# Performance work log

Hardware: AMD Instinct MI355X
Metric: run time of the kernel (lower is better)

The kernel has to match this reference:

```python
import jax, jax.numpy as jnp
import numpy as np

N_NODES = 50000


def setup_inputs() -> dict:
    key = jax.random.key(0)
    ks = jax.random.split(key, 10)
    B, N, D, H, O = 2, N_NODES, 128, 128, 10
    x = jax.random.normal(ks[0], (B, N, D), dtype=jnp.float32)
    edge_index = jax.random.randint(ks[1], (2, 800000), 0, N, dtype=jnp.int32)
    s = lambda fan_in: 1.0 / np.sqrt(fan_in)
    W  = jax.random.uniform(ks[2], (D, H), jnp.float32, -s(D), s(D))
    b  = jnp.zeros((H,), jnp.float32)
    W1 = jax.random.uniform(ks[3], (H, H // 2), jnp.float32, -s(H), s(H))
    b1 = jnp.zeros((H // 2,), jnp.float32)
    W2 = jax.random.uniform(ks[4], (H // 2, H // 4), jnp.float32, -s(H // 2), s(H // 2))
    b2 = jnp.zeros((H // 4,), jnp.float32)
    W3 = jax.random.uniform(ks[5], (H // 4, O), jnp.float32, -s(H // 4), s(H // 4))
    b3 = jnp.zeros((O,), jnp.float32)
    return {"x": x, "edge_index": edge_index, "W": W, "b": b,
            "W1": W1, "b1": b1, "W2": W2, "b2": b2, "W3": W3, "b3": b3}


def reference(x, edge_index, W, b, W1, b1, W2, b2, W3, b3):
    # GraphConvolution (Kipf): support = x @ W; out[dst] += support[src]; + b
    src, dst = edge_index[0], edge_index[1]
    support = jnp.einsum("bnd,dh->bnh", x, W)          # [B, N, H]
    msgs = support[:, src, :]                            # [B, E, H] gather
    agg = jnp.zeros_like(support).at[:, dst, :].add(msgs)  # scatter-add
    h = jax.nn.gelu(agg + b, approximate=False)          # GELU (torch default erf)
    # dropout is identity at inference (training=False)
    h = jax.nn.relu(jnp.einsum("bnh,hk->bnk", h, W1) + b1)
    h = jax.nn.relu(jnp.einsum("bnk,km->bnm", h, W2) + b2)
    h = jnp.einsum("bnm,mo->bno", h, W3) + b3            # [B, N, O]
    return h.mean(axis=1)                                # [B, O]
```

## Files before the change

### kernel.cpp

```cpp
#include <hip/hip_runtime.h>
#include <math.h>

#define NN 50000
#define DD 128
#define HH 128
#define L1 64
#define L2 32
#define OO 10

__device__ __forceinline__ float bf2f_lo(unsigned u) { return __uint_as_float(u << 16); }
__device__ __forceinline__ float bf2f_hi(unsigned u) { return __uint_as_float(u & 0xffff0000u); }
__device__ __forceinline__ unsigned short f2bf(float f) {
    unsigned u = __float_as_uint(f);
    return (unsigned short)((u + 0x7fffu + ((u >> 16) & 1u)) >> 16);
}

__global__ __launch_bounds__(256) void k_support(
    const float* __restrict__ x, const float* __restrict__ W,
    unsigned short* __restrict__ supb, int rows,
    const int* __restrict__ ei, int* __restrict__ counts, int E)
{
    __shared__ float xs[64][DD];
    __shared__ float wh[64][HH];
    const int tid = threadIdx.x;
    const int row0 = blockIdx.x * 64;

    for (int u = tid * 4; u < 64 * DD; u += 256 * 4) {
        const int r = u >> 7, c = u & 127;
        float4 v = make_float4(0.f, 0.f, 0.f, 0.f);
        if (row0 + r < rows) v = *(const float4*)(x + (size_t)(row0 + r) * DD + c);
        *(float4*)(&xs[r][c]) = v;
    }

    {
        const int chunk = (E + gridDim.x - 1) / gridDim.x;
        const int e0 = blockIdx.x * chunk;
        const int e1 = min(e0 + chunk, E);
        for (int e = e0 + tid; e < e1; e += 256)
            atomicAdd(&counts[ei[(size_t)E + e]], 1);
    }

    const int cg = tid & 31;
    const int rg = tid >> 5;
    float4 acc[8];
    #pragma unroll
    for (int i = 0; i < 8; ++i) acc[i] = make_float4(0.f, 0.f, 0.f, 0.f);

    for (int p = 0; p < 2; ++p) {
        __syncthreads();
        for (int u = tid * 4; u < 64 * HH; u += 256 * 4) {
            const int r = u >> 7, c = u & 127;
            *(float4*)(&wh[r][c]) = *(const float4*)(W + (size_t)(p * 64 + r) * HH + c);
        }
        __syncthreads();
        #pragma unroll 2
        for (int k = 0; k < 64; k += 4) {
            float4 wv[4];
            #pragma unroll
            for (int jj = 0; jj < 4; ++jj) wv[jj] = *(const float4*)(&wh[k + jj][cg * 4]);
            #pragma unroll
            for (int q = 0; q < 2; ++q) {
                #pragma unroll
                for (int i = 0; i < 4; ++i) {
                    const float4 xv = *(const float4*)(&xs[q * 32 + rg * 4 + i][p * 64 + k]);
                    float4* a = &acc[q * 4 + i];
                    a->x = fmaf(xv.x, wv[0].x, fmaf(xv.y, wv[1].x, fmaf(xv.z, wv[2].x, fmaf(xv.w, wv[3].x, a->x))));
                    a->y = fmaf(xv.x, wv[0].y, fmaf(xv.y, wv[1].y, fmaf(xv.z, wv[2].y, fmaf(xv.w, wv[3].y, a->y))));
                    a->z = fmaf(xv.x, wv[0].z, fmaf(xv.y, wv[1].z, fmaf(xv.z, wv[2].z, fmaf(xv.w, wv[3].z, a->z))));
                    a->w = fmaf(xv.x, wv[0].w, fmaf(xv.y, wv[1].w, fmaf(xv.z, wv[2].w, fmaf(xv.w, wv[3].w, a->w))));
                }
            }
        }
    }

    #pragma unroll
    for (int q = 0; q < 2; ++q)
        #pragma unroll
        for (int i = 0; i < 4; ++i) {
            const int r = row0 + q * 32 + rg * 4 + i;
            if (r < rows) {
                const float4 a = acc[q * 4 + i];
                ushort4 o;
                o.x = f2bf(a.x); o.y = f2bf(a.y); o.z = f2bf(a.z); o.w = f2bf(a.w);
                *(ushort4*)(supb + (size_t)r * HH + cg * 4) = o;
            }
        }
}

__global__ __launch_bounds__(1024) void k_scan1(
    const int* __restrict__ counts, int* __restrict__ offsets,
    int* __restrict__ blksum, int n)
{
    __shared__ int wsum[16], woff[16];
    const int tid = threadIdx.x, lane = tid & 63, wv = tid >> 6;
    const int i = blockIdx.x * 1024 + tid;
    int v = (i < n) ? counts[i] : 0;
    int x = v;
    #pragma unroll
    for (int d = 1; d < 64; d <<= 1) { int t = __shfl_up(x, d); if (lane >= d) x += t; }
    if (lane == 63) wsum[wv] = x;
    __syncthreads();
    if (wv == 0 && lane < 16) {
        int y = wsum[lane];
        #pragma unroll
        for (int d = 1; d < 16; d <<= 1) { int t = __shfl_up(y, d); if (lane >= d) y += t; }
        woff[lane] = y - wsum[lane];
        if (lane == 15) blksum[blockIdx.x] = y;
    }
    __syncthreads();
    if (i < n) offsets[i] = woff[wv] + (x - v);
}

__global__ __launch_bounds__(1024) void k_scan2(
    int* __restrict__ offsets, const int* __restrict__ blksum, int nblk, int n)
{
    __shared__ int base_sh, tot_sh;
    const int tid = threadIdx.x, lane = tid & 63, wv = tid >> 6;
    if (wv == 0) {
        int v = (lane < nblk) ? blksum[lane] : 0;
        int x = v;
        #pragma unroll
        for (int d = 1; d < 64; d <<= 1) { int t = __shfl_up(x, d); if (lane >= d) x += t; }
        int incl = __shfl(x, blockIdx.x);
        int own  = __shfl(v, blockIdx.x);
        int tot  = __shfl(x, nblk - 1);
        if (lane == 0) { base_sh = incl - own; tot_sh = tot; }
    }
    __syncthreads();
    const int i = blockIdx.x * 1024 + tid;
    if (i < n) offsets[i] += base_sh;
    if (blockIdx.x == nblk - 1 && tid == 0) offsets[n] = tot_sh;
}

__global__ __launch_bounds__(256) void k_bucket(
    const int* __restrict__ ei, const int* __restrict__ offsets,
    int* __restrict__ cursor, int* __restrict__ ss, int E)
{
    int e = blockIdx.x * 256 + threadIdx.x;
    if (e < E) {
        int d = ei[E + e];
        int pos = offsets[d] + atomicAdd(&cursor[d], 1);
        ss[pos] = ei[e];
    }
}

__global__ __launch_bounds__(256) void k_agg(
    const unsigned short* __restrict__ supb, const int* __restrict__ offsets,
    const int* __restrict__ ss, unsigned short* __restrict__ aggb, int nn)
{
    const int tid = threadIdx.x;
    const int lane = tid & 63;
    const int wv = tid >> 6;
    const int d = blockIdx.x * 4 + wv;
    if (d >= nn) return;
    const int b = lane >> 5;
    const int f = lane & 31;
    const size_t bbase = (size_t)b * nn * HH;
    const unsigned short* sp = supb + bbase + f * 4;
    const int s0 = offsets[d], s1 = offsets[d + 1];
    float4 a = make_float4(0.f, 0.f, 0.f, 0.f);
    float4 a2 = make_float4(0.f, 0.f, 0.f, 0.f);
    int i = s0;
    for (; i + 2 <= s1; i += 2) {
        const int sA = ss[i], sB = ss[i + 1];
        const uint2 rA = *(const uint2*)(sp + (size_t)sA * HH);
        const uint2 rB = *(const uint2*)(sp + (size_t)sB * HH);
        a.x  += bf2f_lo(rA.x); a.y  += bf2f_hi(rA.x); a.z  += bf2f_lo(rA.y); a.w  += bf2f_hi(rA.y);
        a2.x += bf2f_lo(rB.x); a2.y += bf2f_hi(rB.x); a2.z += bf2f_lo(rB.y); a2.w += bf2f_hi(rB.y);
    }
    if (i < s1) {
        const uint2 r = *(const uint2*)(sp + (size_t)ss[i] * HH);
        a.x += bf2f_lo(r.x); a.y += bf2f_hi(r.x); a.z += bf2f_lo(r.y); a.w += bf2f_hi(r.y);
    }
    a.x += a2.x; a.y += a2.y; a.z += a2.z; a.w += a2.w;
    ushort4 o;
    o.x = f2bf(a.x); o.y = f2bf(a.y); o.z = f2bf(a.z); o.w = f2bf(a.w);
    *(ushort4*)(aggb + bbase + (size_t)d * HH + f * 4) = o;
}

__global__ __launch_bounds__(256) void k_scatter(
    const int* __restrict__ ei, const unsigned short* __restrict__ supb,
    float* __restrict__ aggf, int E, int B)
{
    const int tid = threadIdx.x;
    const int eg = tid >> 5;
    const int t4 = (tid & 31) << 2;
    const int e = blockIdx.x * 8 + eg;
    if (e >= E) return;
    const int src = ei[e];
    const int dst = ei[E + e];
    for (int b = 0; b < B; ++b) {
        const uint2 r = *(const uint2*)(supb + ((size_t)b * NN + src) * HH + t4);
        float* ap = aggf + ((size_t)b * NN + dst) * HH + t4;
        unsafeAtomicAdd(ap + 0, bf2f_lo(r.x));
        unsafeAtomicAdd(ap + 1, bf2f_hi(r.x));
        unsafeAtomicAdd(ap + 2, bf2f_lo(r.y));
        unsafeAtomicAdd(ap + 3, bf2f_hi(r.y));
    }
}

__global__ __launch_bounds__(256) void k_cvt(
    const float* __restrict__ in, unsigned short* __restrict__ outb, int n)
{
    int i = blockIdx.x * 256 + threadIdx.x;
    if (i < n) outb[i] = f2bf(in[i]);
}

__global__ __launch_bounds__(512) void k_mlp(
    const unsigned short* __restrict__ aggb, const float* __restrict__ b0v,
    const float* __restrict__ W1, const float* __restrict__ b1v,
    const float* __restrict__ W2, const float* __restrict__ b2v,
    float* __restrict__ partials, int rows)
{
    __shared__ float w1s[HH][L1];
    __shared__ float w2s[L1][L2];
    __shared__ float hs[64 * 136];
    __shared__ float b0s[DD], b1s[L1], b2s[L2];
    __shared__ float oacc[64];

    const int tid = threadIdx.x;
    const int row0 = blockIdx.x * 64;

    for (int u = tid * 4; u < HH * L1; u += 2048)
        *(float4*)(&w1s[u >> 6][u & 63]) = *(const float4*)(W1 + u);
    for (int u = tid * 4; u < L1 * L2; u += 2048)
        *(float4*)(&w2s[u >> 5][u & 31]) = *(const float4*)(W2 + u);
    if (tid < DD) b0s[tid] = b0v[tid];
    if (tid < L1) b1s[tid] = b1v[tid];
    if (tid < L2) b2s[tid] = b2v[tid];
    if (tid < 64) oacc[tid] = 0.f;
    __syncthreads();

    for (int u = tid * 8; u < 64 * DD; u += 512 * 8) {
        const int r = u >> 7, c = u & 127;
        float4 g0 = make_float4(0.f, 0.f, 0.f, 0.f);
        float4 g1 = g0;
        if (row0 + r < rows) {
            const uint4 raw = *(const uint4*)(aggb + (size_t)(row0 + r) * HH + c);
            float v[8];
            v[0] = bf2f_lo(raw.x) + b0s[c + 0]; v[1] = bf2f_hi(raw.x) + b0s[c + 1];
            v[2] = bf2f_lo(raw.y) + b0s[c + 2]; v[3] = bf2f_hi(raw.y) + b0s[c + 3];
            v[4] = bf2f_lo(raw.z) + b0s[c + 4]; v[5] = bf2f_hi(raw.z) + b0s[c + 5];
            v[6] = bf2f_lo(raw.w) + b0s[c + 6]; v[7] = bf2f_hi(raw.w) + b0s[c + 7];
            #pragma unroll
            for (int t = 0; t < 8; ++t) v[t] = 0.5f * v[t] * (1.f + erff(v[t] * 0.70710678118654752f));
            g0 = make_float4(v[0], v[1], v[2], v[3]);
            g1 = make_float4(v[4], v[5], v[6], v[7]);
        }
        *(float4*)(&hs[r * 136 + c]) = g0;
        *(float4*)(&hs[r * 136 + c + 4]) = g1;
    }
    __syncthreads();

    const int cg = tid & 15;
    const int rg = tid >> 4;
    float4 acc0 = *(const float4*)(&b1s[cg * 4]);
    float4 acc1 = acc0;
    #pragma unroll 4
    for (int j = 0; j < HH; j += 4) {
        float4 wv[4];
        #pragma unroll
        for (int jj = 0; jj < 4; ++jj) wv[jj] = *(const float4*)(&w1s[j + jj][cg * 4]);
        const float4 h0 = *(const float4*)(&hs[(rg * 2 + 0) * 136 + j]);
        const float4 h1 = *(const float4*)(&hs[(rg * 2 + 1) * 136 + j]);
        acc0.x = fmaf(h0.x, wv[0].x, fmaf(h0.y, wv[1].x, fmaf(h0.z, wv[2].x, fmaf(h0.w, wv[3].x, acc0.x))));
        acc0.y = fmaf(h0.x, wv[0].y, fmaf(h0.y, wv[1].y, fmaf(h0.z, wv[2].y, fmaf(h0.w, wv[3].y, acc0.y))));
        acc0.z = fmaf(h0.x, wv[0].z, fmaf(h0.y, wv[1].z, fmaf(h0.z, wv[2].z, fmaf(h0.w, wv[3].z, acc0.z))));
        acc0.w = fmaf(h0.x, wv[0].w, fmaf(h0.y, wv[1].w, fmaf(h0.z, wv[2].w, fmaf(h0.w, wv[3].w, acc0.w))));
        acc1.x = fmaf(h1.x, wv[0].x, fmaf(h1.y, wv[1].x, fmaf(h1.z, wv[2].x, fmaf(h1.w, wv[3].x, acc1.x))));
        acc1.y = fmaf(h1.x, wv[0].y, fmaf(h1.y, wv[1].y, fmaf(h1.z, wv[2].y, fmaf(h1.w, wv[3].y, acc1.y))));
        acc1.z = fmaf(h1.x, wv[0].z, fmaf(h1.y, wv[1].z, fmaf(h1.z, wv[2].z, fmaf(h1.w, wv[3].z, acc1.z))));
        acc1.w = fmaf(h1.x, wv[0].w, fmaf(h1.y, wv[1].w, fmaf(h1.z, wv[2].w, fmaf(h1.w, wv[3].w, acc1.w))));
    }
    acc0.x = fmaxf(acc0.x, 0.f); acc0.y = fmaxf(acc0.y, 0.f);
    acc0.z = fmaxf(acc0.z, 0.f); acc0.w = fmaxf(acc0.w, 0.f);
    acc1.x = fmaxf(acc1.x, 0.f); acc1.y = fmaxf(acc1.y, 0.f);
    acc1.z = fmaxf(acc1.z, 0.f); acc1.w = fmaxf(acc1.w, 0.f);
    __syncthreads();
    float* h1p = hs;
    *(float4*)(&h1p[(rg * 2 + 0) * 68 + cg * 4]) = acc0;
    *(float4*)(&h1p[(rg * 2 + 1) * 68 + cg * 4]) = acc1;
    __syncthreads();

    float* h2p = hs + 5120;
    {
        const int cg2 = tid & 7;
        const int r2 = tid >> 3;
        float4 a = *(const float4*)(&b2s[cg2 * 4]);
        #pragma unroll 4
        for (int j = 0; j < L1; j += 4) {
            float4 wv[4];
            #pragma unroll
            for (int jj = 0; jj < 4; ++jj) wv[jj] = *(const float4*)(&w2s[j + jj][cg2 * 4]);
            const float4 hv = *(const float4*)(&h1p[r2 * 68 + j]);
            a.x = fmaf(hv.x, wv[0].x, fmaf(hv.y, wv[1].x, fmaf(hv.z, wv[2].x, fmaf(hv.w, wv[3].x, a.x))));
            a.y = fmaf(hv.x, wv[0].y, fmaf(hv.y, wv[1].y, fmaf(hv.z, wv[2].y, fmaf(hv.w, wv[3].y, a.y))));
            a.z = fmaf(hv.x, wv[0].z, fmaf(hv.y, wv[1].z, fmaf(hv.z, wv[2].z, fmaf(hv.w, wv[3].z, a.z))));
            a.w = fmaf(hv.x, wv[0].w, fmaf(hv.y, wv[1].w, fmaf(hv.z, wv[2].w, fmaf(hv.w, wv[3].w, a.w))));
        }
        a.x = fmaxf(a.x, 0.f); a.y = fmaxf(a.y, 0.f);
        a.z = fmaxf(a.z, 0.f); a.w = fmaxf(a.w, 0.f);
        __syncthreads();
        *(float4*)(&h2p[r2 * 36 + cg2 * 4]) = a;
    }
    __syncthreads();

    {
        const int c = tid & 31;
        const int g = tid >> 5;
        float p0 = 0.f, p1 = 0.f;
        #pragma unroll
        for (int i = 0; i < 4; ++i) {
            const int r = g * 4 + i;
            const int grow = row0 + r;
            if (grow < rows) {
                const float v = h2p[r * 36 + c];
                if (grow >= NN) p1 += v; else p0 += v;
            }
        }
        if (p0 != 0.f) atomicAdd(&oacc[c], p0);
        if (p1 != 0.f) atomicAdd(&oacc[32 + c], p1);
    }
    __syncthreads();
    if (tid < 64) partials[(size_t)blockIdx.x * 64 + tid] = oacc[tid];
}

__global__ __launch_bounds__(256) void k_reduce(
    const float* __restrict__ partials, float* __restrict__ accum, int nblk)
{
    __shared__ float lsum[4][64];
    const int t = threadIdx.x & 63;
    const int w = threadIdx.x >> 6;
    float s = 0.f;
    for (int g = blockIdx.x * 4 + w; g < nblk; g += gridDim.x * 4)
        s += partials[(size_t)g * 64 + t];
    lsum[w][t] = s;
    __syncthreads();
    if (threadIdx.x < 64) {
        const float v = lsum[0][t] + lsum[1][t] + lsum[2][t] + lsum[3][t];
        unsafeAtomicAdd(&accum[t], v);
    }
}

__global__ __launch_bounds__(64) void k_final(
    const float* __restrict__ accum, const float* __restrict__ W3,
    const float* __restrict__ b3v, float* __restrict__ out)
{
    const int tid = threadIdx.x;
    if (tid < 2 * OO) {
        const int b = tid / OO, o = tid % OO;
        float acc = b3v[o];
        const float inv = 1.0f / (float)NN;
        #pragma unroll
        for (int j = 0; j < L2; ++j) acc += (accum[b * 32 + j] * inv) * W3[j * OO + o];
        out[tid] = acc;
    }
}

extern "C" void kernel_launch(void* const* d_in, const int* in_sizes, int n_in,
                              void* d_out, int out_size, void* d_ws, size_t ws_size,
                              hipStream_t stream) {
    const float* x  = (const float*)d_in[0];
    const int*   ei = (const int*)d_in[1];
    const float* W  = (const float*)d_in[2];
    const float* b0 = (const float*)d_in[3];
    const float* W1 = (const float*)d_in[4];
    const float* b1 = (const float*)d_in[5];
    const float* W2 = (const float*)d_in[6];
    const float* b2 = (const float*)d_in[7];
    const float* W3 = (const float*)d_in[8];
    const float* b3 = (const float*)d_in[9];
    float* out = (float*)d_out;

    const int B = in_sizes[0] / (NN * DD);
    const int E = in_sizes[1] / 2;
    const int rows = B * NN;
    const int nblk_mlp = (rows + 63) / 64;
    const int nsb = (NN + 1023) / 1024;

    unsigned short* supb = (unsigned short*)d_ws;
    unsigned short* aggb = supb + (size_t)rows * HH;
    float* partials = (float*)(aggb + (size_t)rows * HH);
    float* accum    = partials + (size_t)nblk_mlp * 64;
    int*   counts   = (int*)(accum + 64);
    int*   cursor   = counts + NN;
    int*   offsets  = cursor + NN;
    int*   blksum   = offsets + NN + 1;
    int*   ss       = blksum + 64;
    const size_t need = ((size_t)rows * HH * 2) * sizeof(unsigned short)
                      + ((size_t)nblk_mlp * 64 + 64) * sizeof(float)
                      + ((size_t)NN * 3 + 1 + 64 + E) * sizeof(int);

    if (ws_size >= need && nsb <= 64) {
        hipMemsetAsync(accum, 0, (64 + 2 * (size_t)NN) * sizeof(int), stream);
        k_support<<<dim3(nblk_mlp), dim3(256), 0, stream>>>(x, W, supb, rows, ei, counts, E);
        k_scan1<<<dim3(nsb), dim3(1024), 0, stream>>>(counts, offsets, blksum, NN);
        k_scan2<<<dim3(nsb), dim3(1024), 0, stream>>>(offsets, blksum, nsb, NN);
        k_bucket<<<dim3((E + 255) / 256), dim3(256), 0, stream>>>(ei, offsets, cursor, ss, E);
        k_agg<<<dim3((NN + 3) / 4), dim3(256), 0, stream>>>(supb, offsets, ss, aggb, NN);
    } else {
        float* aggf = (float*)counts;
        hipMemsetAsync(accum, 0, 64 * sizeof(float), stream);
        hipMemsetAsync(aggf, 0, (size_t)rows * HH * sizeof(float), stream);
        k_support<<<dim3(nblk_mlp), dim3(256), 0, stream>>>(x, W, supb, rows, ei, (int*)aggf, 0);
        k_scatter<<<dim3((E + 7) / 8), dim3(256), 0, stream>>>(ei, supb, aggf, E, B);
        k_cvt<<<dim3((rows * HH + 255) / 256), dim3(256), 0, stream>>>(aggf, aggb, rows * HH);
    }

    k_mlp<<<dim3(nblk_mlp), dim3(512), 0, stream>>>(aggb, b0, W1, b1, W2, b2, partials, rows);
    k_reduce<<<dim3(64), dim3(256), 0, stream>>>(partials, accum, nblk_mlp);
    k_final<<<dim3(1), dim3(64), 0, stream>>>(accum, W3, b3, out);
}
```

Before: 322.0 us.

## Fuse CSR aggregation with GELU and MLP; read W directly in support GEMM

The CSR gather-aggregation now writes GELU activations straight into shared memory and runs the two hidden MLP layers plus the partial mean in the same kernel. This removes the bf16 agg buffer round trip through global memory and one kernel launch. The support GEMM also drops its shared-memory staging of W and reads W from global (L1/L2-cached) memory, with a launch-bounds occupancy hint, which frees LDS. The fused kernel is larger, so fewer blocks may fit per CU and gather latency may be harder to hide. The fallback path now feeds fp32 agg directly into the MLP instead of converting to bf16 first.

After: 363.5 us. 12.9% more time.

```diff
diff --git a/kernel.cpp b/kernel.cpp
--- a/kernel.cpp
+++ b/kernel.cpp
@@ -14,14 +14,16 @@
     unsigned u = __float_as_uint(f);
     return (unsigned short)((u + 0x7fffu + ((u >> 16) & 1u)) >> 16);
 }
-
-__global__ __launch_bounds__(256) void k_support(
+__device__ __forceinline__ float gelu_f(float v) {
+    return 0.5f * v * (1.f + erff(v * 0.70710678118654752f));
+}
+
+__global__ __launch_bounds__(256, 4) void k_support(
     const float* __restrict__ x, const float* __restrict__ W,
     unsigned short* __restrict__ supb, int rows,
     const int* __restrict__ ei, int* __restrict__ counts, int E)
 {
     __shared__ float xs[64][DD];
-    __shared__ float wh[64][HH];
     const int tid = threadIdx.x;
     const int row0 = blockIdx.x * 64;
 
@@ -45,30 +47,24 @@
     float4 acc[8];
     #pragma unroll
     for (int i = 0; i < 8; ++i) acc[i] = make_float4(0.f, 0.f, 0.f, 0.f);
-
-    for (int p = 0; p < 2; ++p) {
-        __syncthreads();
-        for (int u = tid * 4; u < 64 * HH; u += 256 * 4) {
-            const int r = u >> 7, c = u & 127;
-            *(float4*)(&wh[r][c]) = *(const float4*)(W + (size_t)(p * 64 + r) * HH + c);
-        }
-        __syncthreads();
-        #pragma unroll 2
-        for (int k = 0; k < 64; k += 4) {
-            float4 wv[4];
+    __syncthreads();
+
+    const float* wp = W + cg * 4;
+    #pragma unroll 2
+    for (int k = 0; k < DD; k += 4) {
+        float4 wv[4];
+        #pragma unroll
+        for (int jj = 0; jj < 4; ++jj) wv[jj] = *(const float4*)(wp + (size_t)(k + jj) * HH);
+        #pragma unroll
+        for (int q = 0; q < 2; ++q) {
             #pragma unroll
-            for (int jj = 0; jj < 4; ++jj) wv[jj] = *(const float4*)(&wh[k + jj][cg * 4]);
-            #pragma unroll
-            for (int q = 0; q < 2; ++q) {
-                #pragma unroll
-                for (int i = 0; i < 4; ++i) {
-                    const float4 xv = *(const float4*)(&xs[q * 32 + rg * 4 + i][p * 64 + k]);
-                    float4* a = &acc[q * 4 + i];
-                    a->x = fmaf(xv.x, wv[0].x, fmaf(xv.y, wv[1].x, fmaf(xv.z, wv[2].x, fmaf(xv.w, wv[3].x, a->x))));
-                    a->y = fmaf(xv.x, wv[0].y, fmaf(xv.y, wv[1].y, fmaf(xv.z, wv[2].y, fmaf(xv.w, wv[3].y, a->y))));
-                    a->z = fmaf(xv.x, wv[0].z, fmaf(xv.y, wv[1].z, fmaf(xv.z, wv[2].z, fmaf(xv.w, wv[3].z, a->z))));
-                    a->w = fmaf(xv.x, wv[0].w, fmaf(xv.y, wv[1].w, fmaf(xv.z, wv[2].w, fmaf(xv.w, wv[3].w, a->w))));
-                }
+            for (int i = 0; i < 4; ++i) {
+                const float4 xv = *(const float4*)(&xs[q * 32 + rg * 4 + i][k]);
+                float4* a = &acc[q * 4 + i];
+                a->x = fmaf(xv.x, wv[0].x, fmaf(xv.y, wv[1].x, fmaf(xv.z, wv[2].x, fmaf(xv.w, wv[3].x, a->x))));
+                a->y = fmaf(xv.x, wv[0].y, fmaf(xv.y, wv[1].y, fmaf(xv.z, wv[2].y, fmaf(xv.w, wv[3].y, a->y))));
+                a->z = fmaf(xv.x, wv[0].z, fmaf(xv.y, wv[1].z, fmaf(xv.z, wv[2].z, fmaf(xv.w, wv[3].z, a->z))));
+                a->w = fmaf(xv.x, wv[0].w, fmaf(xv.y, wv[1].w, fmaf(xv.z, wv[2].w, fmaf(xv.w, wv[3].w, a->w))));
             }
         }
     }
@@ -144,38 +140,140 @@
     }
 }
 
-__global__ __launch_bounds__(256) void k_agg(
+__global__ __launch_bounds__(512) void k_aggmlp(
     const unsigned short* __restrict__ supb, const int* __restrict__ offsets,
-    const int* __restrict__ ss, unsigned short* __restrict__ aggb, int nn)
-{
+    const int* __restrict__ ss, const float* __restrict__ b0v,
+    const float* __restrict__ W1, const float* __restrict__ b1v,
+    const float* __restrict__ W2, const float* __restrict__ b2v,
+    float* __restrict__ partials, int nn)
+{
+    __shared__ float w1s[HH][L1];
+    __shared__ float w2s[L1][L2];
+    __shared__ float hs[64 * 136];
+    __shared__ float b0s[DD], b1s[L1], b2s[L2];
+    __shared__ float oacc[64];
+
     const int tid = threadIdx.x;
-    const int lane = tid & 63;
-    const int wv = tid >> 6;
-    const int d = blockIdx.x * 4 + wv;
-    if (d >= nn) return;
-    const int b = lane >> 5;
-    const int f = lane & 31;
-    const size_t bbase = (size_t)b * nn * HH;
-    const unsigned short* sp = supb + bbase + f * 4;
-    const int s0 = offsets[d], s1 = offsets[d + 1];
-    float4 a = make_float4(0.f, 0.f, 0.f, 0.f);
-    float4 a2 = make_float4(0.f, 0.f, 0.f, 0.f);
-    int i = s0;
-    for (; i + 2 <= s1; i += 2) {
-        const int sA = ss[i], sB = ss[i + 1];
-        const uint2 rA = *(const uint2*)(sp + (size_t)sA * HH);
-        const uint2 rB = *(const uint2*)(sp + (size_t)sB * HH);
-        a.x  += bf2f_lo(rA.x); a.y  += bf2f_hi(rA.x); a.z  += bf2f_lo(rA.y); a.w  += bf2f_hi(rA.y);
-        a2.x += bf2f_lo(rB.x); a2.y += bf2f_hi(rB.x); a2.z += bf2f_lo(rB.y); a2.w += bf2f_hi(rB.y);
-    }
-    if (i < s1) {
-        const uint2 r = *(const uint2*)(sp + (size_t)ss[i] * HH);
-        a.x += bf2f_lo(r.x); a.y += bf2f_hi(r.x); a.z += bf2f_lo(r.y); a.w += bf2f_hi(r.y);
-    }
-    a.x += a2.x; a.y += a2.y; a.z += a2.z; a.w += a2.w;
-    ushort4 o;
-    o.x = f2bf(a.x); o.y = f2bf(a.y); o.z = f2bf(a.z); o.w = f2bf(a.w);
-    *(ushort4*)(aggb + bbase + (size_t)d * HH + f * 4) = o;
+    const int d0 = blockIdx.x * 32;
+
+    for (int u = tid * 4; u < HH * L1; u += 2048)
+        *(float4*)(&w1s[u >> 6][u & 63]) = *(const float4*)(W1 + u);
+    for (int u = tid * 4; u < L1 * L2; u += 2048)
+        *(float4*)(&w2s[u >> 5][u & 31]) = *(const float4*)(W2 + u);
+    if (tid < DD) b0s[tid] = b0v[tid];
+    if (tid < L1) b1s[tid] = b1v[tid];
+    if (tid < L2) b2s[tid] = b2v[tid];
+    if (tid < 64) oacc[tid] = 0.f;
+    __syncthreads();
+
+    {
+        const int lane = tid & 63;
+        const int wv = tid >> 6;
+        const int b = lane >> 5;
+        const int f = lane & 31;
+        const unsigned short* sp = supb + (size_t)b * nn * HH + f * 4;
+        #pragma unroll
+        for (int i4 = 0; i4 < 4; ++i4) {
+            const int dl = wv * 4 + i4;
+            const int d = d0 + dl;
+            float4 a = make_float4(0.f, 0.f, 0.f, 0.f);
+            float4 a2 = make_float4(0.f, 0.f, 0.f, 0.f);
+            if (d < nn) {
+                const int s0 = offsets[d], s1 = offsets[d + 1];
+                int i = s0;
+                for (; i + 2 <= s1; i += 2) {
+                    const int sA = ss[i], sB = ss[i + 1];
+                    const uint2 rA = *(const uint2*)(sp + (size_t)sA * HH);
+                    const uint2 rB = *(const uint2*)(sp + (size_t)sB * HH);
+                    a.x  += bf2f_lo(rA.x); a.y  += bf2f_hi(rA.x); a.z  += bf2f_lo(rA.y); a.w  += bf2f_hi(rA.y);
+                    a2.x += bf2f_lo(rB.x); a2.y += bf2f_hi(rB.x); a2.z += bf2f_lo(rB.y); a2.w += bf2f_hi(rB.y);
+                }
+                if (i < s1) {
+                    const uint2 r = *(const uint2*)(sp + (size_t)ss[i] * HH);
+                    a.x += bf2f_lo(r.x); a.y += bf2f_hi(r.x); a.z += bf2f_lo(r.y); a.w += bf2f_hi(r.y);
+                }
+            }
+            const float4 bb = *(const float4*)(&b0s[f * 4]);
+            float4 g;
+            g.x = gelu_f(a.x + a2.x + bb.x);
+            g.y = gelu_f(a.y + a2.y + bb.y);
+            g.z = gelu_f(a.z + a2.z + bb.z);
+            g.w = gelu_f(a.w + a2.w + bb.w);
+            *(float4*)(&hs[(b * 32 + dl) * 136 + f * 4]) = g;
+        }
+    }
+    __syncthreads();
+
+    const int cg = tid & 15;
+    const int rg = tid >> 4;
+    float4 acc0 = *(const float4*)(&b1s[cg * 4]);
+    float4 acc1 = acc0;
+    #pragma unroll 4
+    for (int j = 0; j < HH; j += 4) {
+        float4 wv[4];
+        #pragma unroll
+        for (int jj = 0; jj < 4; ++jj) wv[jj] = *(const float4*)(&w1s[j + jj][cg * 4]);
+        const float4 h0 = *(const float4*)(&hs[(rg * 2 + 0) * 136 + j]);
+        const float4 h1 = *(const float4*)(&hs[(rg * 2 + 1) * 136 + j]);
+        acc0.x = fmaf(h0.x, wv[0].x, fmaf(h0.y, wv[1].x, fmaf(h0.z, wv[2].x, fmaf(h0.w, wv[3].x, acc0.x))));
+        acc0.y = fmaf(h0.x, wv[0].y, fmaf(h0.y, wv[1].y, fmaf(h0.z, wv[2].y, fmaf(h0.w, wv[3].y, acc0.y))));
+        acc0.z = fmaf(h0.x, wv[0].z, fmaf(h0.y, wv[1].z, fmaf(h0.z, wv[2].z, fmaf(h0.w, wv[3].z, acc0.z))));
+        acc0.w = fmaf(h0.x, wv[0].w, fmaf(h0.y, wv[1].w, fmaf(h0.z, wv[2].w, fmaf(h0.w, wv[3].w, acc0.w))));
+        acc1.x = fmaf(h1.x, wv[0].x, fmaf(h1.y, wv[1].x, fmaf(h1.z, wv[2].x, fmaf(h1.w, wv[3].x, acc1.x))));
+        acc1.y = fmaf(h1.x, wv[0].y, fmaf(h1.y, wv[1].y, fmaf(h1.z, wv[2].y, fmaf(h1.w, wv[3].y, acc1.y))));
+        acc1.z = fmaf(h1.x, wv[0].z, fmaf(h1.y, wv[1].z, fmaf(h1.z, wv[2].z, fmaf(h1.w, wv[3].z, acc1.z))));
+        acc1.w = fmaf(h1.x, wv[0].w, fmaf(h1.y, wv[1].w, fmaf(h1.z, wv[2].w, fmaf(h1.w, wv[3].w, acc1.w))));
+    }
+    acc0.x = fmaxf(acc0.x, 0.f); acc0.y = fmaxf(acc0.y, 0.f);
+    acc0.z = fmaxf(acc0.z, 0.f); acc0.w = fmaxf(acc0.w, 0.f);
+    acc1.x = fmaxf(acc1.x, 0.f); acc1.y = fmaxf(acc1.y, 0.f);
+    acc1.z = fmaxf(acc1.z, 0.f); acc1.w = fmaxf(acc1.w, 0.f);
+    __syncthreads();
+    float* h1p = hs;
+    *(float4*)(&h1p[(rg * 2 + 0) * 68 + cg * 4]) = acc0;
+    *(float4*)(&h1p[(rg * 2 + 1) * 68 + cg * 4]) = acc1;
+    __syncthreads();
+
+    float* h2p = hs + 5120;
+    {
+        const int cg2 = tid & 7;
+        const int r2 = tid >> 3;
+        float4 a = *(const float4*)(&b2s[cg2 * 4]);
+        #pragma unroll 4
+        for (int j = 0; j < L1; j += 4) {
+            float4 wv[4];
+            #pragma unroll
+            for (int jj = 0; jj < 4; ++jj) wv[jj] = *(const float4*)(&w2s[j + jj][cg2 * 4]);
+            const float4 hv = *(const float4*)(&h1p[r2 * 68 + j]);
+            a.x = fmaf(hv.x, wv[0].x, fmaf(hv.y, wv[1].x, fmaf(hv.z, wv[2].x, fmaf(hv.w, wv[3].x, a.x))));
+            a.y = fmaf(hv.x, wv[0].y, fmaf(hv.y, wv[1].y, fmaf(hv.z, wv[2].y, fmaf(hv.w, wv[3].y, a.y))));
+            a.z = fmaf(hv.x, wv[0].z, fmaf(hv.y, wv[1].z, fmaf(hv.z, wv[2].z, fmaf(hv.w, wv[3].z, a.z))));
+            a.w = fmaf(hv.x, wv[0].w, fmaf(hv.y, wv[1].w, fmaf(hv.z, wv[2].w, fmaf(hv.w, wv[3].w, a.w))));
+        }
+        a.x = fmaxf(a.x, 0.f); a.y = fmaxf(a.y, 0.f);
+        a.z = fmaxf(a.z, 0.f); a.w = fmaxf(a.w, 0.f);
+        __syncthreads();
+        *(float4*)(&h2p[r2 * 36 + cg2 * 4]) = a;
+    }
+    __syncthreads();
+
+    {
+        const int c = tid & 31;
+        const int g = tid >> 5;
+        float p0 = 0.f, p1 = 0.f;
+        #pragma unroll
+        for (int i = 0; i < 4; ++i) {
+            const int r = g * 4 + i;
+            if (d0 + (r & 31) < nn) {
+                const float v = h2p[r * 36 + c];
+                if (r >= 32) p1 += v; else p0 += v;
+            }
+        }
+        if (p0 != 0.f) atomicAdd(&oacc[c], p0);
+        if (p1 != 0.f) atomicAdd(&oacc[32 + c], p1);
+    }
+    __syncthreads();
+    if (tid < 64) partials[(size_t)blockIdx.x * 64 + tid] = oacc[tid];
 }
 
 __global__ __launch_bounds__(256) void k_scatter(
@@ -199,15 +297,8 @@
     }
 }
 
-__global__ __launch_bounds__(256) void k_cvt(
-    const float* __restrict__ in, unsigned short* __restrict__ outb, int n)
-{
-    int i = blockIdx.x * 256 + threadIdx.x;
-    if (i < n) outb[i] = f2bf(in[i]);
-}
-
-__global__ __launch_bounds__(512) void k_mlp(
-    const unsigned short* __restrict__ aggb, const float* __restrict__ b0v,
+__global__ __launch_bounds__(512) void k_mlp_g(
+    const float* __restrict__ aggf, const float* __restrict__ b0v,
     const float* __restrict__ W1, const float* __restrict__ b1v,
     const float* __restrict__ W2, const float* __restrict__ b2v,
     float* __restrict__ partials, int rows)
@@ -231,24 +322,15 @@
     if (tid < 64) oacc[tid] = 0.f;
     __syncthreads();
 
-    for (int u = tid * 8; u < 64 * DD; u += 512 * 8) {
+    for (int u = tid * 4; u < 64 * DD; u += 2048) {
         const int r = u >> 7, c = u & 127;
-        float4 g0 = make_float4(0.f, 0.f, 0.f, 0.f);
-        float4 g1 = g0;
+        float4 g = make_float4(0.f, 0.f, 0.f, 0.f);
         if (row0 + r < rows) {
-            const uint4 raw = *(const uint4*)(aggb + (size_t)(row0 + r) * HH + c);
-            float v[8];
-            v[0] = bf2f_lo(raw.x) + b0s[c + 0]; v[1] = bf2f_hi(raw.x) + b0s[c + 1];
-            v[2] = bf2f_lo(raw.y) + b0s[c + 2]; v[3] = bf2f_hi(raw.y) + b0s[c + 3];
-            v[4] = bf2f_lo(raw.z) + b0s[c + 4]; v[5] = bf2f_hi(raw.z) + b0s[c + 5];
-            v[6] = bf2f_lo(raw.w) + b0s[c + 6]; v[7] = bf2f_hi(raw.w) + b0s[c + 7];
-            #pragma unroll
-            for (int t = 0; t < 8; ++t) v[t] = 0.5f * v[t] * (1.f + erff(v[t] * 0.70710678118654752f));
-            g0 = make_float4(v[0], v[1], v[2], v[3]);
-            g1 = make_float4(v[4], v[5], v[6], v[7]);
-        }
-        *(float4*)(&hs[r * 136 + c]) = g0;
-        *(float4*)(&hs[r * 136 + c + 4]) = g1;
+            const float4 v = *(const float4*)(aggf + (size_t)(row0 + r) * HH + c);
+            g.x = gelu_f(v.x + b0s[c + 0]); g.y = gelu_f(v.y + b0s[c + 1]);
+            g.z = gelu_f(v.z + b0s[c + 2]); g.w = gelu_f(v.w + b0s[c + 3]);
+        }
+        *(float4*)(&hs[r * 136 + c]) = g;
     }
     __syncthreads();
 
@@ -256,7 +338,6 @@
     const int rg = tid >> 4;
     float4 acc0 = *(const float4*)(&b1s[cg * 4]);
     float4 acc1 = acc0;
-    #pragma unroll 4
     for (int j = 0; j < HH; j += 4) {
         float4 wv[4];
         #pragma unroll
@@ -287,7 +368,6 @@
         const int cg2 = tid & 7;
         const int r2 = tid >> 3;
         float4 a = *(const float4*)(&b2s[cg2 * 4]);
-        #pragma unroll 4
         for (int j = 0; j < L1; j += 4) {
             float4 wv[4];
             #pragma unroll
@@ -375,39 +455,38 @@
     const int B = in_sizes[0] / (NN * DD);
     const int E = in_sizes[1] / 2;
     const int rows = B * NN;
-    const int nblk_mlp = (rows + 63) / 64;
+    const int nblk = (NN + 31) / 32;
     const int nsb = (NN + 1023) / 1024;
 
     unsigned short* supb = (unsigned short*)d_ws;
-    unsigned short* aggb = supb + (size_t)rows * HH;
-    float* partials = (float*)(aggb + (size_t)rows * HH);
-    float* accum    = partials + (size_t)nblk_mlp * 64;
+    float* partials = (float*)(supb + (size_t)rows * HH);
+    float* accum    = partials + (size_t)nblk * 64;
     int*   counts   = (int*)(accum + 64);
     int*   cursor   = counts + NN;
     int*   offsets  = cursor + NN;
     int*   blksum   = offsets + NN + 1;
     int*   ss       = blksum + 64;
-    const size_t need = ((size_t)rows * HH * 2) * sizeof(unsigned short)
-                      + ((size_t)nblk_mlp * 64 + 64) * sizeof(float)
+    float* aggf     = (float*)(ss + E);
+    const size_t need_csr = ((size_t)rows * HH) * sizeof(unsigned short)
+                      + ((size_t)nblk * 64 + 64) * sizeof(float)
                       + ((size_t)NN * 3 + 1 + 64 + E) * sizeof(int);
-
-    if (ws_size >= need && nsb <= 64) {
+    const size_t need_fb = need_csr + (size_t)rows * HH * sizeof(float);
+
+    if (ws_size >= need_csr && nsb <= 64) {
         hipMemsetAsync(accum, 0, (64 + 2 * (size_t)NN) * sizeof(int), stream);
-        k_support<<<dim3(nblk_mlp), dim3(256), 0, stream>>>(x, W, supb, rows, ei, counts, E);
+        k_support<<<dim3((rows + 63) / 64), dim3(256), 0, stream>>>(x, W, supb, rows, ei, counts, E);
         k_scan1<<<dim3(nsb), dim3(1024), 0, stream>>>(counts, offsets, blksum, NN);
         k_scan2<<<dim3(nsb), dim3(1024), 0, stream>>>(offsets, blksum, nsb, NN);
         k_bucket<<<dim3((E + 255) / 256), dim3(256), 0, stream>>>(ei, offsets, cursor, ss, E);
-        k_agg<<<dim3((NN + 3) / 4), dim3(256), 0, stream>>>(supb, offsets, ss, aggb, NN);
-    } else {
-        float* aggf = (float*)counts;
+        k_aggmlp<<<dim3(nblk), dim3(512), 0, stream>>>(supb, offsets, ss, b0, W1, b1, W2, b2, partials, NN);
+    } else if (ws_size >= need_fb) {
         hipMemsetAsync(accum, 0, 64 * sizeof(float), stream);
         hipMemsetAsync(aggf, 0, (size_t)rows * HH * sizeof(float), stream);
-        k_support<<<dim3(nblk_mlp), dim3(256), 0, stream>>>(x, W, supb, rows, ei, (int*)aggf, 0);
+        k_support<<<dim3((rows + 63) / 64), dim3(256), 0, stream>>>(x, W, supb, rows, ei, counts, 0);
         k_scatter<<<dim3((E + 7) / 8), dim3(256), 0, stream>>>(ei, supb, aggf, E, B);
-        k_cvt<<<dim3((rows * HH + 255) / 256), dim3(256), 0, stream>>>(aggf, aggb, rows * HH);
-    }
-
-    k_mlp<<<dim3(nblk_mlp), dim3(512), 0, stream>>>(aggb, b0, W1, b1, W2, b2, partials, rows);
-    k_reduce<<<dim3(64), dim3(256), 0, stream>>>(partials, accum, nblk_mlp);
+        k_mlp_g<<<dim3(nblk), dim3(512), 0, stream>>>(aggf, b0, W1, b1, W2, b2, partials, rows);
+    }
+
+    k_reduce<<<dim3(64), dim3(256), 0, stream>>>(partials, accum, nblk);
     k_final<<<dim3(1), dim3(64), 0, stream>>>(accum, W3, b3, out);
 }
```

## Interleave batch rows in support layout and read W directly from global

Applied to the files above, without the earlier changes.

The support matrix is now stored with node-major, batch-interleaved rows, so the two batch copies of each node sit in one contiguous 512-byte row. The aggregation wave then gathers both batches with a single 64-lane contiguous load per source, and the gather loop is unrolled to four sources. k_support no longer stages W in shared memory and reads it straight from global/L1 under a tighter launch bound. The MLP reduction infers the batch from row parity, and the fallback path now gets its own workspace region; this hardcodes B=2 and may add global-load latency in the GEMM.

After: 314.8 us. -2.2%, faster.

```diff
diff --git a/kernel.cpp b/kernel.cpp
--- a/kernel.cpp
+++ b/kernel.cpp
@@ -14,14 +14,16 @@
     unsigned u = __float_as_uint(f);
     return (unsigned short)((u + 0x7fffu + ((u >> 16) & 1u)) >> 16);
 }
-
-__global__ __launch_bounds__(256) void k_support(
+__device__ __forceinline__ float gelu_f(float v) {
+    return 0.5f * v * (1.f + erff(v * 0.70710678118654752f));
+}
+
+__global__ __launch_bounds__(256, 4) void k_support(
     const float* __restrict__ x, const float* __restrict__ W,
     unsigned short* __restrict__ supb, int rows,
     const int* __restrict__ ei, int* __restrict__ counts, int E)
 {
     __shared__ float xs[64][DD];
-    __shared__ float wh[64][HH];
     const int tid = threadIdx.x;
     const int row0 = blockIdx.x * 64;
 
@@ -45,30 +47,24 @@
     float4 acc[8];
     #pragma unroll
     for (int i = 0; i < 8; ++i) acc[i] = make_float4(0.f, 0.f, 0.f, 0.f);
-
-    for (int p = 0; p < 2; ++p) {
-        __syncthreads();
-        for (int u = tid * 4; u < 64 * HH; u += 256 * 4) {
-            const int r = u >> 7, c = u & 127;
-            *(float4*)(&wh[r][c]) = *(const float4*)(W + (size_t)(p * 64 + r) * HH + c);
-        }
-        __syncthreads();
-        #pragma unroll 2
-        for (int k = 0; k < 64; k += 4) {
-            float4 wv[4];
+    __syncthreads();
+
+    const float* wp = W + cg * 4;
+    #pragma unroll 2
+    for (int k = 0; k < DD; k += 4) {
+        float4 wv[4];
+        #pragma unroll
+        for (int jj = 0; jj < 4; ++jj) wv[jj] = *(const float4*)(wp + (size_t)(k + jj) * HH);
+        #pragma unroll
+        for (int q = 0; q < 2; ++q) {
             #pragma unroll
-            for (int jj = 0; jj < 4; ++jj) wv[jj] = *(const float4*)(&wh[k + jj][cg * 4]);
-            #pragma unroll
-            for (int q = 0; q < 2; ++q) {
-                #pragma unroll
-                for (int i = 0; i < 4; ++i) {
-                    const float4 xv = *(const float4*)(&xs[q * 32 + rg * 4 + i][p * 64 + k]);
-                    float4* a = &acc[q * 4 + i];
-                    a->x = fmaf(xv.x, wv[0].x, fmaf(xv.y, wv[1].x, fmaf(xv.z, wv[2].x, fmaf(xv.w, wv[3].x, a->x))));
-                    a->y = fmaf(xv.x, wv[0].y, fmaf(xv.y, wv[1].y, fmaf(xv.z, wv[2].y, fmaf(xv.w, wv[3].y, a->y))));
-                    a->z = fmaf(xv.x, wv[0].z, fmaf(xv.y, wv[1].z, fmaf(xv.z, wv[2].z, fmaf(xv.w, wv[3].z, a->z))));
-                    a->w = fmaf(xv.x, wv[0].w, fmaf(xv.y, wv[1].w, fmaf(xv.z, wv[2].w, fmaf(xv.w, wv[3].w, a->w))));
-                }
+            for (int i = 0; i < 4; ++i) {
+                const float4 xv = *(const float4*)(&xs[q * 32 + rg * 4 + i][k]);
+                float4* a = &acc[q * 4 + i];
+                a->x = fmaf(xv.x, wv[0].x, fmaf(xv.y, wv[1].x, fmaf(xv.z, wv[2].x, fmaf(xv.w, wv[3].x, a->x))));
+                a->y = fmaf(xv.x, wv[0].y, fmaf(xv.y, wv[1].y, fmaf(xv.z, wv[2].y, fmaf(xv.w, wv[3].y, a->y))));
+                a->z = fmaf(xv.x, wv[0].z, fmaf(xv.y, wv[1].z, fmaf(xv.z, wv[2].z, fmaf(xv.w, wv[3].z, a->z))));
+                a->w = fmaf(xv.x, wv[0].w, fmaf(xv.y, wv[1].w, fmaf(xv.z, wv[2].w, fmaf(xv.w, wv[3].w, a->w))));
             }
         }
     }
@@ -79,10 +75,13 @@
         for (int i = 0; i < 4; ++i) {
             const int r = row0 + q * 32 + rg * 4 + i;
             if (r < rows) {
+                const int b = (r >= NN) ? 1 : 0;
+                const int n = r - b * NN;
+                const size_t sr = (size_t)n * 2 + b;
                 const float4 a = acc[q * 4 + i];
                 ushort4 o;
                 o.x = f2bf(a.x); o.y = f2bf(a.y); o.z = f2bf(a.z); o.w = f2bf(a.w);
-                *(ushort4*)(supb + (size_t)r * HH + cg * 4) = o;
+                *(ushort4*)(supb + sr * HH + cg * 4) = o;
             }
         }
 }
@@ -153,64 +152,37 @@
     const int wv = tid >> 6;
     const int d = blockIdx.x * 4 + wv;
     if (d >= nn) return;
-    const int b = lane >> 5;
-    const int f = lane & 31;
-    const size_t bbase = (size_t)b * nn * HH;
-    const unsigned short* sp = supb + bbase + f * 4;
+    const unsigned short* sp = supb + lane * 4;
     const int s0 = offsets[d], s1 = offsets[d + 1];
     float4 a = make_float4(0.f, 0.f, 0.f, 0.f);
     float4 a2 = make_float4(0.f, 0.f, 0.f, 0.f);
     int i = s0;
-    for (; i + 2 <= s1; i += 2) {
-        const int sA = ss[i], sB = ss[i + 1];
-        const uint2 rA = *(const uint2*)(sp + (size_t)sA * HH);
-        const uint2 rB = *(const uint2*)(sp + (size_t)sB * HH);
+    for (; i + 4 <= s1; i += 4) {
+        const int sA = ss[i], sB = ss[i + 1], sC = ss[i + 2], sD = ss[i + 3];
+        const uint2 rA = *(const uint2*)(sp + (size_t)sA * 256);
+        const uint2 rB = *(const uint2*)(sp + (size_t)sB * 256);
+        const uint2 rC = *(const uint2*)(sp + (size_t)sC * 256);
+        const uint2 rD = *(const uint2*)(sp + (size_t)sD * 256);
         a.x  += bf2f_lo(rA.x); a.y  += bf2f_hi(rA.x); a.z  += bf2f_lo(rA.y); a.w  += bf2f_hi(rA.y);
         a2.x += bf2f_lo(rB.x); a2.y += bf2f_hi(rB.x); a2.z += bf2f_lo(rB.y); a2.w += bf2f_hi(rB.y);
-    }
-    if (i < s1) {
-        const uint2 r = *(const uint2*)(sp + (size_t)ss[i] * HH);
+        a.x  += bf2f_lo(rC.x); a.y  += bf2f_hi(rC.x); a.z  += bf2f_lo(rC.y); a.w  += bf2f_hi(rC.y);
+        a2.x += bf2f_lo(rD.x); a2.y += bf2f_hi(rD.x); a2.z += bf2f_lo(rD.y); a2.w += bf2f_hi(rD.y);
+    }
+    for (; i < s1; ++i) {
+        const uint2 r = *(const uint2*)(sp + (size_t)ss[i] * 256);
         a.x += bf2f_lo(r.x); a.y += bf2f_hi(r.x); a.z += bf2f_lo(r.y); a.w += bf2f_hi(r.y);
     }
     a.x += a2.x; a.y += a2.y; a.z += a2.z; a.w += a2.w;
     ushort4 o;
     o.x = f2bf(a.x); o.y = f2bf(a.y); o.z = f2bf(a.z); o.w = f2bf(a.w);
-    *(ushort4*)(aggb + bbase + (size_t)d * HH + f * 4) = o;
-}
-
-__global__ __launch_bounds__(256) void k_scatter(
-    const int* __restrict__ ei, const unsigned short* __restrict__ supb,
-    float* __restrict__ aggf, int E, int B)
-{
-    const int tid = threadIdx.x;
-    const int eg = tid >> 5;
-    const int t4 = (tid & 31) << 2;
-    const int e = blockIdx.x * 8 + eg;
-    if (e >= E) return;
-    const int src = ei[e];
-    const int dst = ei[E + e];
-    for (int b = 0; b < B; ++b) {
-        const uint2 r = *(const uint2*)(supb + ((size_t)b * NN + src) * HH + t4);
-        float* ap = aggf + ((size_t)b * NN + dst) * HH + t4;
-        unsafeAtomicAdd(ap + 0, bf2f_lo(r.x));
-        unsafeAtomicAdd(ap + 1, bf2f_hi(r.x));
-        unsafeAtomicAdd(ap + 2, bf2f_lo(r.y));
-        unsafeAtomicAdd(ap + 3, bf2f_hi(r.y));
-    }
-}
-
-__global__ __launch_bounds__(256) void k_cvt(
-    const float* __restrict__ in, unsigned short* __restrict__ outb, int n)
-{
-    int i = blockIdx.x * 256 + threadIdx.x;
-    if (i < n) outb[i] = f2bf(in[i]);
+    *(ushort4*)(aggb + (size_t)d * 256 + lane * 4) = o;
 }
 
 __global__ __launch_bounds__(512) void k_mlp(
     const unsigned short* __restrict__ aggb, const float* __restrict__ b0v,
     const float* __restrict__ W1, const float* __restrict__ b1v,
     const float* __restrict__ W2, const float* __restrict__ b2v,
-    float* __restrict__ partials, int rows)
+    float* __restrict__ partials, int srows)
 {
     __shared__ float w1s[HH][L1];
     __shared__ float w2s[L1][L2];
@@ -235,7 +207,7 @@
         const int r = u >> 7, c = u & 127;
         float4 g0 = make_float4(0.f, 0.f, 0.f, 0.f);
         float4 g1 = g0;
-        if (row0 + r < rows) {
+        if (row0 + r < srows) {
             const uint4 raw = *(const uint4*)(aggb + (size_t)(row0 + r) * HH + c);
             float v[8];
             v[0] = bf2f_lo(raw.x) + b0s[c + 0]; v[1] = bf2f_hi(raw.x) + b0s[c + 1];
@@ -243,7 +215,7 @@
             v[4] = bf2f_lo(raw.z) + b0s[c + 4]; v[5] = bf2f_hi(raw.z) + b0s[c + 5];
             v[6] = bf2f_lo(raw.w) + b0s[c + 6]; v[7] = bf2f_hi(raw.w) + b0s[c + 7];
             #pragma unroll
-            for (int t = 0; t < 8; ++t) v[t] = 0.5f * v[t] * (1.f + erff(v[t] * 0.70710678118654752f));
+            for (int t = 0; t < 8; ++t) v[t] = gelu_f(v[t]);
             g0 = make_float4(v[0], v[1], v[2], v[3]);
             g1 = make_float4(v[4], v[5], v[6], v[7]);
         }
@@ -312,10 +284,9 @@
         #pragma unroll
         for (int i = 0; i < 4; ++i) {
             const int r = g * 4 + i;
-            const int grow = row0 + r;
-            if (grow < rows) {
+            if (row0 + r < srows) {
                 const float v = h2p[r * 36 + c];
-                if (grow >= NN) p1 += v; else p0 += v;
+                if (r & 1) p1 += v; else p0 += v;
             }
         }
         if (p0 != 0.f) atomicAdd(&oacc[c], p0);
@@ -323,6 +294,32 @@
     }
     __syncthreads();
     if (tid < 64) partials[(size_t)blockIdx.x * 64 + tid] = oacc[tid];
+}
+
+__global__ __launch_bounds__(256) void k_scatter(
+    const int* __restrict__ ei, const unsigned short* __restrict__ supb,
+    float* __restrict__ aggf, int E)
+{
+    const int tid = threadIdx.x;
+    const int eg = tid >> 6;
+    const int lane = tid & 63;
+    const int e = blockIdx.x * 4 + eg;
+    if (e >= E) return;
+    const int src = ei[e];
+    const int dst = ei[E + e];
+    const uint2 r = *(const uint2*)(supb + (size_t)src * 256 + lane * 4);
+    float* ap = aggf + (size_t)dst * 256 + lane * 4;
+    unsafeAtomicAdd(ap + 0, bf2f_lo(r.x));
+    unsafeAtomicAdd(ap + 1, bf2f_hi(r.x));
+    unsafeAtomicAdd(ap + 2, bf2f_lo(r.y));
+    unsafeAtomicAdd(ap + 3, bf2f_hi(r.y));
+}
+
+__global__ __launch_bounds__(256) void k_cvt(
+    const float* __restrict__ in, unsigned short* __restrict__ outb, int n)
+{
+    int i = blockIdx.x * 256 + threadIdx.x;
+    if (i < n) outb[i] = f2bf(in[i]);
 }
 
 __global__ __launch_bounds__(256) void k_reduce(
@@ -372,42 +369,43 @@
     const float* b3 = (const float*)d_in[9];
     float* out = (float*)d_out;
 
-    const int B = in_sizes[0] / (NN * DD);
     const int E = in_sizes[1] / 2;
-    const int rows = B * NN;
-    const int nblk_mlp = (rows + 63) / 64;
+    const int rows = 2 * NN;
+    const int nblk = (rows + 63) / 64;
     const int nsb = (NN + 1023) / 1024;
 
     unsigned short* supb = (unsigned short*)d_ws;
     unsigned short* aggb = supb + (size_t)rows * HH;
     float* partials = (float*)(aggb + (size_t)rows * HH);
-    float* accum    = partials + (size_t)nblk_mlp * 64;
+    float* accum    = partials + (size_t)nblk * 64;
     int*   counts   = (int*)(accum + 64);
     int*   cursor   = counts + NN;
     int*   offsets  = cursor + NN;
     int*   blksum   = offsets + NN + 1;
     int*   ss       = blksum + 64;
-    const size_t need = ((size_t)rows * HH * 2) * sizeof(unsigned short)
-                      + ((size_t)nblk_mlp * 64 + 64) * sizeof(float)
+    float* aggf     = (float*)(ss + E);
+    const size_t need_csr = ((size_t)rows * HH * 2) * sizeof(unsigned short)
+                      + ((size_t)nblk * 64 + 64) * sizeof(float)
                       + ((size_t)NN * 3 + 1 + 64 + E) * sizeof(int);
-
-    if (ws_size >= need && nsb <= 64) {
+    const size_t need_fb = need_csr + (size_t)rows * HH * sizeof(float);
+
+    if (ws_size >= need_csr && nsb <= 64) {
         hipMemsetAsync(accum, 0, (64 + 2 * (size_t)NN) * sizeof(int), stream);
-        k_support<<<dim3(nblk_mlp), dim3(256), 0, stream>>>(x, W, supb, rows, ei, counts, E);
+        k_support<<<dim3((rows + 63) / 64), dim3(256), 0, stream>>>(x, W, supb, rows, ei, counts, E);
         k_scan1<<<dim3(nsb), dim3(1024), 0, stream>>>(counts, offsets, blksum, NN);
         k_scan2<<<dim3(nsb), dim3(1024), 0, stream>>>(offsets, blksum, nsb, NN);
         k_bucket<<<dim3((E + 255) / 256), dim3(256), 0, stream>>>(ei, offsets, cursor, ss, E);
         k_agg<<<dim3((NN + 3) / 4), dim3(256), 0, stream>>>(supb, offsets, ss, aggb, NN);
-    } else {
-        float* aggf = (float*)counts;
+        k_mlp<<<dim3(nblk), dim3(512), 0, stream>>>(aggb, b0, W1, b1, W2, b2, partials, rows);
+    } else if (ws_size >= need_fb) {
         hipMemsetAsync(accum, 0, 64 * sizeof(float), stream);
         hipMemsetAsync(aggf, 0, (size_t)rows * HH * sizeof(float), stream);
-        k_support<<<dim3(nblk_mlp), dim3(256), 0, stream>>>(x, W, supb, rows, ei, (int*)aggf, 0);
-        k_scatter<<<dim3((E + 7) / 8), dim3(256), 0, stream>>>(ei, supb, aggf, E, B);
+        k_support<<<dim3((rows + 63) / 64), dim3(256), 0, stream>>>(x, W, supb, rows, ei, counts, 0);
+        k_scatter<<<dim3((E + 3) / 4), dim3(256), 0, stream>>>(ei, supb, aggf, E);
         k_cvt<<<dim3((rows * HH + 255) / 256), dim3(256), 0, stream>>>(aggf, aggb, rows * HH);
-    }
-
-    k_mlp<<<dim3(nblk_mlp), dim3(512), 0, stream>>>(aggb, b0, W1, b1, W2, b2, partials, rows);
-    k_reduce<<<dim3(64), dim3(256), 0, stream>>>(partials, accum, nblk_mlp);
+        k_mlp<<<dim3(nblk), dim3(512), 0, stream>>>(aggb, b0, W1, b1, W2, b2, partials, rows);
+    }
+
+    k_reduce<<<dim3(64), dim3(256), 0, stream>>>(partials, accum, nblk);
     k_final<<<dim3(1), dim3(64), 0, stream>>>(accum, W3, b3, out);
 }
```
